# Kernel tuning notes

Hardware: AMD Instinct MI355X
Metric: run time of the kernel (lower is better)

## Reference

```python
import jax, jax.numpy as jnp
import numpy as np

B, S, D, P = 8, 2048, 512, 64  # batch, seq, num_embed_hidden, num_attention_project


def setup_inputs() -> dict:
    key = jax.random.key(0)
    ks = jax.random.split(key, 9)
    sd = 1.0 / np.sqrt(D)
    sp = 1.0 / np.sqrt(P)
    return {
        "query": jax.random.normal(ks[0], (B, S, D), dtype=jnp.float32),
        "attention_mask": jnp.ones((B, S), dtype=jnp.float32),
        "Wq": jax.random.uniform(ks[1], (D, P), jnp.float32, -sd, sd),
        "bq": jax.random.uniform(ks[2], (P,), jnp.float32, -sd, sd),
        "Wk": jax.random.uniform(ks[3], (D, P), jnp.float32, -sd, sd),
        "bk": jax.random.uniform(ks[4], (P,), jnp.float32, -sd, sd),
        "Wv": jax.random.uniform(ks[5], (D, P), jnp.float32, -sd, sd),
        "bv": jax.random.uniform(ks[6], (P,), jnp.float32, -sd, sd),
        "Wo": jax.random.uniform(ks[7], (P, D), jnp.float32, -sp, sp),
        "bo": jax.random.uniform(ks[8], (D,), jnp.float32, -sp, sp),
    }


def reference(query, attention_mask, Wq, bq, Wk, bk, Wv, bv, Wo, bo):
    q = jnp.einsum("bsd,dp->bsp", query, Wq) + bq  # [B,S,P]
    k = jnp.einsum("bsd,dp->bsp", query, Wk) + bk
    v = jnp.einsum("bsd,dp->bsp", query, Wv) + bv
    scores = jnp.einsum("bsp,btp->bst", q, k) / jnp.sqrt(jnp.float32(P))  # [B,S,S]
    # Faithful to original: mask broadcast over last axis via unsqueeze(-1) -> masks rows
    scores = scores + (1.0 - attention_mask[:, :, None]) * -10000.0
    weights = jax.nn.softmax(scores, axis=-1)
    weighted = jnp.einsum("bst,btp->bsp", weights, v)
    return jnp.einsum("bsp,pd->bsd", weighted, Wo) + bo
```

## Files before the change

### kernel.cpp

```cpp
#include <hip/hip_runtime.h>
#include <hip/hip_bf16.h>
#include <math.h>

constexpr int B = 8;
constexpr int S = 2048;
constexpr int D = 512;
constexpr int P = 64;
constexpr float SCALE = 0.125f;

typedef short bf16x8 __attribute__((ext_vector_type(8)));
typedef float f32x4 __attribute__((ext_vector_type(4)));
typedef unsigned int u32;

__device__ __forceinline__ unsigned short f2bf(float x) {
  __hip_bfloat16 h = __float2bfloat16(x);
  return __builtin_bit_cast(unsigned short, h);
}
__device__ __forceinline__ float bf2f(unsigned short u) {
  unsigned int v = (unsigned int)u << 16;
  return __builtin_bit_cast(float, v);
}

__device__ __forceinline__ void ld_g2lds16(const unsigned short* g,
                                           unsigned short* l) {
  __builtin_amdgcn_global_load_lds(
      (const __attribute__((address_space(1))) u32*)g,
      (__attribute__((address_space(3))) u32*)l, 16, 0, 0);
}

__global__ __launch_bounds__(256) void prep_w(
    const float* __restrict__ Wq, const float* __restrict__ Wk,
    const float* __restrict__ Wv, const float* __restrict__ Wo,
    unsigned short* __restrict__ WcatT, unsigned short* __restrict__ WoT) {
  const int i = blockIdx.x * 256 + threadIdx.x;
  if (i < 192 * 512) {
    const int n = i >> 9, k = i & 511;
    const float* W = (n < 64) ? Wq : (n < 128) ? Wk : Wv;
    WcatT[i] = f2bf(W[k * 64 + (n & 63)]);
  }
  if (i < 512 * 64) {
    WoT[i] = f2bf(Wo[(i & 63) * 512 + (i >> 6)]);
  }
}

__global__ __launch_bounds__(256) void qkv_mfma(
    const float* __restrict__ query, const unsigned short* __restrict__ WcatT,
    const float* __restrict__ bq, const float* __restrict__ bk,
    const float* __restrict__ bv, unsigned short* __restrict__ q_bf,
    unsigned short* __restrict__ k_bf, unsigned short* __restrict__ vT_bf) {
  __shared__ __align__(16) unsigned short Aq[64 * 512];
  __shared__ __align__(16) unsigned short Bb[192 * 64];

  const int tid = threadIdx.x;
  const int w = tid >> 6;
  const int l = tid & 63;
  const int l15 = l & 15;
  const int l4 = l >> 4;
  const int s0 = blockIdx.x * 64;

  const float* qsrc = query + (size_t)s0 * D;
  for (int step = 0; step < 16; ++step) {
    const int row = step * 4 + w;
    const float* pf = qsrc + row * D + l * 8;
    const float4 x = *(const float4*)pf;
    const float4 y = *(const float4*)(pf + 4);
    bf16x8 u;
    u[0] = (short)f2bf(x.x); u[1] = (short)f2bf(x.y);
    u[2] = (short)f2bf(x.z); u[3] = (short)f2bf(x.w);
    u[4] = (short)f2bf(y.x); u[5] = (short)f2bf(y.y);
    u[6] = (short)f2bf(y.z); u[7] = (short)f2bf(y.w);
    *(bf16x8*)&Aq[row * 512 + ((l ^ (row & 7)) << 3)] = u;
  }

  f32x4 acc[4][3];
#pragma unroll
  for (int st = 0; st < 4; ++st)
#pragma unroll
    for (int nt = 0; nt < 3; ++nt) acc[st][nt] = (f32x4){0.f, 0.f, 0.f, 0.f};

  const int wn = w * 48;

  for (int kc = 0; kc < 8; ++kc) {
#pragma unroll
    for (int c = 0; c < 6; ++c) {
      const int n = c * 32 + w * 8 + (l >> 3);
      const unsigned short* gp =
          WcatT + (size_t)n * 512 + kc * 64 + (((l & 7) ^ (l >> 3)) << 3);
      ld_g2lds16(gp, &Bb[(c * 256 + w * 64) * 8]);
    }
    __syncthreads();

#pragma unroll
    for (int kk = 0; kk < 2; ++kk) {
      bf16x8 af[4], bfr[3];
#pragma unroll
      for (int st = 0; st < 4; ++st) {
        const int row = st * 16 + l15;
        const int slot = (kc * 8 + kk * 4 + l4) ^ (row & 7);
        af[st] = *(const bf16x8*)&Aq[row * 512 + (slot << 3)];
      }
#pragma unroll
      for (int nt = 0; nt < 3; ++nt) {
        const int n = wn + nt * 16 + l15;
        const int slot = (kk * 4 + l4) ^ (n & 7);
        bfr[nt] = *(const bf16x8*)&Bb[n * 64 + (slot << 3)];
      }
#pragma unroll
      for (int st = 0; st < 4; ++st)
#pragma unroll
        for (int nt = 0; nt < 3; ++nt)
          acc[st][nt] = __builtin_amdgcn_mfma_f32_16x16x32_bf16(
              af[st], bfr[nt], acc[st][nt], 0, 0, 0);
    }
    __syncthreads();
  }

  const int batch = s0 >> 11;
  const int sloc = s0 & 2047;
#pragma unroll
  for (int st = 0; st < 4; ++st) {
#pragma unroll
    for (int nt = 0; nt < 3; ++nt) {
      const int col = wn + nt * 16 + l15;
      const int mat = col >> 6;
      const int p = col & 63;
      const float bb = ((mat == 0) ? bq : (mat == 1) ? bk : bv)[p];
#pragma unroll
      for (int r = 0; r < 4; ++r) {
        const int row = st * 16 + l4 * 4 + r;
        const float vl = acc[st][nt][r] + bb;
        if (mat == 0)
          q_bf[(size_t)(s0 + row) * P + p] = f2bf(vl * SCALE);
        else if (mat == 1)
          k_bf[(size_t)(s0 + row) * P + p] = f2bf(vl);
        else
          vT_bf[((size_t)batch * P + p) * S + sloc + row] = f2bf(vl);
      }
    }
  }
}

__global__ __launch_bounds__(256) void attn(
    const unsigned short* __restrict__ q_bf,
    const unsigned short* __restrict__ k_bf,
    const unsigned short* __restrict__ vT_bf,
    unsigned short* __restrict__ wout) {
  __shared__ __align__(16) unsigned short e_lds[4][2][16 * 32];
  __shared__ __align__(16) float wacc_lds[4][32 * 64];
  __shared__ float l_lds[4][32];

  const int tid = threadIdx.x;
  const int w = tid >> 6;
  const int lane = tid & 63;
  const int l15 = lane & 15;
  const int l4 = lane >> 4;

  const int blk = blockIdx.x;
  const int b = blk & 7;
  const int qt = blk >> 3;
  const int s0 = qt * 32;

  const unsigned short* qb = q_bf + ((size_t)b * S + s0) * P;
  const unsigned short* kb = k_bf + (size_t)b * S * P;
  const unsigned short* vtb = vT_bf + (size_t)b * P * S;

  bf16x8 aq[2][2];
#pragma unroll
  for (int st = 0; st < 2; ++st)
#pragma unroll
    for (int h = 0; h < 2; ++h)
      aq[st][h] =
          *(const bf16x8*)(qb + (size_t)(st * 16 + l15) * P + h * 32 + l4 * 8);

  f32x4 acc[2][4];
#pragma unroll
  for (int st = 0; st < 2; ++st)
#pragma unroll
    for (int pc = 0; pc < 4; ++pc) acc[st][pc] = (f32x4){0.f, 0.f, 0.f, 0.f};
  float lpart[2][4] = {{0.f, 0.f, 0.f, 0.f}, {0.f, 0.f, 0.f, 0.f}};

  for (int win = 0; win < 16; ++win) {
    const int t0 = w * 512 + win * 32;

    bf16x8 bk[2][2];
#pragma unroll
    for (int tile = 0; tile < 2; ++tile)
#pragma unroll
      for (int h = 0; h < 2; ++h)
        bk[tile][h] = *(const bf16x8*)(kb +
                                       (size_t)(t0 + tile * 16 + l15) * P +
                                       h * 32 + l4 * 8);

#pragma unroll
    for (int st = 0; st < 2; ++st) {
#pragma unroll
      for (int tile = 0; tile < 2; ++tile) {
        f32x4 c = (f32x4){0.f, 0.f, 0.f, 0.f};
        c = __builtin_amdgcn_mfma_f32_16x16x32_bf16(aq[st][0], bk[tile][0], c,
                                                    0, 0, 0);
        c = __builtin_amdgcn_mfma_f32_16x16x32_bf16(aq[st][1], bk[tile][1], c,
                                                    0, 0, 0);
#pragma unroll
        for (int r = 0; r < 4; ++r) {
          const unsigned short eu = f2bf(__expf(c[r]));
          lpart[st][r] += bf2f(eu);
          e_lds[w][st][(l4 * 4 + r) * 32 + tile * 16 + l15] = eu;
        }
      }
    }

#pragma unroll
    for (int st = 0; st < 2; ++st) {
      const bf16x8 ae = *(const bf16x8*)&e_lds[w][st][l15 * 32 + l4 * 8];
#pragma unroll
      for (int pc = 0; pc < 4; ++pc) {
        const bf16x8 bv = *(const bf16x8*)(vtb +
                                           (size_t)(pc * 16 + l15) * S + t0 +
                                           l4 * 8);
        acc[st][pc] =
            __builtin_amdgcn_mfma_f32_16x16x32_bf16(ae, bv, acc[st][pc], 0, 0,
                                                    0);
      }
    }
  }

#pragma unroll
  for (int st = 0; st < 2; ++st) {
#pragma unroll
    for (int r = 0; r < 4; ++r) {
      float v = lpart[st][r];
      v += __shfl_xor(v, 1, 64);
      v += __shfl_xor(v, 2, 64);
      v += __shfl_xor(v, 4, 64);
      v += __shfl_xor(v, 8, 64);
      if (l15 == 0) l_lds[w][st * 16 + l4 * 4 + r] = v;
    }
  }

#pragma unroll
  for (int st = 0; st < 2; ++st)
#pragma unroll
    for (int pc = 0; pc < 4; ++pc)
#pragma unroll
      for (int r = 0; r < 4; ++r)
        wacc_lds[w][(st * 16 + l4 * 4 + r) * 64 + pc * 16 + l15] =
            acc[st][pc][r];
  __syncthreads();

  for (int i = tid; i < 32 * 64; i += 256) {
    const int row = i >> 6;
    const int p = i & 63;
    float s = 0.f, ls = 0.f;
#pragma unroll
    for (int ww = 0; ww < 4; ++ww) {
      s += wacc_lds[ww][row * 64 + p];
      ls += l_lds[ww][row];
    }
    wout[((size_t)b * S + s0 + row) * P + p] = f2bf(s / ls);
  }
}

__global__ __launch_bounds__(256) void out_mfma(
    const unsigned short* __restrict__ wtd,
    const unsigned short* __restrict__ WoT,
    const float* __restrict__ bo, float* __restrict__ out) {
  __shared__ __align__(16) unsigned short Aw[64 * 64];
  __shared__ __align__(16) unsigned short Bo[128 * 64];

  const int tid = threadIdx.x;
  const int w = tid >> 6;
  const int l = tid & 63;
  const int l15 = l & 15;
  const int l4 = l >> 4;
  const int s0 = (blockIdx.x >> 2) * 64;
  const int nb = (blockIdx.x & 3) * 128;

#pragma unroll
  for (int c = 0; c < 2; ++c) {
    const int row = c * 32 + w * 8 + (l >> 3);
    const unsigned short* gp =
        wtd + (size_t)(s0 + row) * 64 + (((l & 7) ^ (l >> 3)) << 3);
    ld_g2lds16(gp, &Aw[(c * 256 + w * 64) * 8]);
  }
#pragma unroll
  for (int c = 0; c < 4; ++c) {
    const int n = c * 32 + w * 8 + (l >> 3);
    const unsigned short* gp =
        WoT + (size_t)(nb + n) * 64 + (((l & 7) ^ (l >> 3)) << 3);
    ld_g2lds16(gp, &Bo[(c * 256 + w * 64) * 8]);
  }
  __syncthreads();

  f32x4 acc[4][2];
#pragma unroll
  for (int st = 0; st < 4; ++st)
#pragma unroll
    for (int nt = 0; nt < 2; ++nt) acc[st][nt] = (f32x4){0.f, 0.f, 0.f, 0.f};

#pragma unroll
  for (int kk = 0; kk < 2; ++kk) {
    bf16x8 af[4], bfr[2];
#pragma unroll
    for (int st = 0; st < 4; ++st) {
      const int row = st * 16 + l15;
      const int slot = (kk * 4 + l4) ^ (row & 7);
      af[st] = *(const bf16x8*)&Aw[row * 64 + (slot << 3)];
    }
#pragma unroll
    for (int nt = 0; nt < 2; ++nt) {
      const int n = w * 32 + nt * 16 + l15;
      const int slot = (kk * 4 + l4) ^ (n & 7);
      bfr[nt] = *(const bf16x8*)&Bo[n * 64 + (slot << 3)];
    }
#pragma unroll
    for (int st = 0; st < 4; ++st)
#pragma unroll
      for (int nt = 0; nt < 2; ++nt)
        acc[st][nt] = __builtin_amdgcn_mfma_f32_16x16x32_bf16(
            af[st], bfr[nt], acc[st][nt], 0, 0, 0);
  }

#pragma unroll
  for (int st = 0; st < 4; ++st) {
#pragma unroll
    for (int nt = 0; nt < 2; ++nt) {
      const int col = nb + w * 32 + nt * 16 + l15;
      const float bb = bo[col];
#pragma unroll
      for (int r = 0; r < 4; ++r) {
        const int row = st * 16 + l4 * 4 + r;
        out[(size_t)(s0 + row) * D + col] = acc[st][nt][r] + bb;
      }
    }
  }
}

extern "C" void kernel_launch(void* const* d_in, const int* in_sizes, int n_in,
                              void* d_out, int out_size, void* d_ws,
                              size_t ws_size, hipStream_t stream) {
  const float* query = (const float*)d_in[0];
  const float* Wq = (const float*)d_in[2];
  const float* bq = (const float*)d_in[3];
  const float* Wk = (const float*)d_in[4];
  const float* bk = (const float*)d_in[5];
  const float* Wv = (const float*)d_in[6];
  const float* bv = (const float*)d_in[7];
  const float* Wo = (const float*)d_in[8];
  const float* bo = (const float*)d_in[9];
  float* out = (float*)d_out;

  const size_t n_rows = (size_t)B * S;
  const size_t proj = n_rows * P;
  unsigned short* qbf = (unsigned short*)d_ws;
  unsigned short* kbf = qbf + proj;
  unsigned short* vtbf = kbf + proj;
  unsigned short* wtd = vtbf + proj;
  unsigned short* WcatT = wtd + proj;
  unsigned short* WoT = WcatT + 192 * 512;

  prep_w<<<384, 256, 0, stream>>>(Wq, Wk, Wv, Wo, WcatT, WoT);
  qkv_mfma<<<256, 256, 0, stream>>>(query, WcatT, bq, bk, bv, qbf, kbf, vtbf);
  attn<<<512, 256, 0, stream>>>(qbf, kbf, vtbf, wtd);
  out_mfma<<<1024, 256, 0, stream>>>(wtd, WoT, bo, out);
}
```

Measured before the change: 151.2 us.

## Fuse output projection into attention and retile QKV projection kernel

Merges the output-projection GEMM into the attention kernel, so the normalized weighted values are written to LDS as bf16 and multiplied by WoT in the same block. This drops the intermediate global buffer and one launch. The attention kernel now handles 16 query rows per block (1024 blocks), swizzles the exp tile in LDS and prefetches the next K window into registers. The QKV kernel uses 32-row tiles with 512 blocks and reads weights straight from global memory instead of staging them through LDS. Each attention block now rereads all of WoT, and removing the weight staging adds uncached global traffic.

```diff
diff --git a/kernel.cpp b/kernel.cpp
--- a/kernel.cpp
+++ b/kernel.cpp
@@ -19,13 +19,6 @@
 __device__ __forceinline__ float bf2f(unsigned short u) {
   unsigned int v = (unsigned int)u << 16;
   return __builtin_bit_cast(float, v);
-}
-
-__device__ __forceinline__ void ld_g2lds16(const unsigned short* g,
-                                           unsigned short* l) {
-  __builtin_amdgcn_global_load_lds(
-      (const __attribute__((address_space(1))) u32*)g,
-      (__attribute__((address_space(3))) u32*)l, 16, 0, 0);
 }
 
 __global__ __launch_bounds__(256) void prep_w(
@@ -43,23 +36,22 @@
   }
 }
 
-__global__ __launch_bounds__(256) void qkv_mfma(
+__global__ __launch_bounds__(256, 2) void qkv_mfma(
     const float* __restrict__ query, const unsigned short* __restrict__ WcatT,
     const float* __restrict__ bq, const float* __restrict__ bk,
     const float* __restrict__ bv, unsigned short* __restrict__ q_bf,
     unsigned short* __restrict__ k_bf, unsigned short* __restrict__ vT_bf) {
-  __shared__ __align__(16) unsigned short Aq[64 * 512];
-  __shared__ __align__(16) unsigned short Bb[192 * 64];
+  __shared__ __align__(16) unsigned short Aq[32 * 512];
 
   const int tid = threadIdx.x;
   const int w = tid >> 6;
   const int l = tid & 63;
   const int l15 = l & 15;
   const int l4 = l >> 4;
-  const int s0 = blockIdx.x * 64;
+  const int s0 = blockIdx.x * 32;
 
   const float* qsrc = query + (size_t)s0 * D;
-  for (int step = 0; step < 16; ++step) {
+  for (int step = 0; step < 8; ++step) {
     const int row = step * 4 + w;
     const float* pf = qsrc + row * D + l * 8;
     const float4 x = *(const float4*)pf;
@@ -71,54 +63,47 @@
     u[6] = (short)f2bf(y.z); u[7] = (short)f2bf(y.w);
     *(bf16x8*)&Aq[row * 512 + ((l ^ (row & 7)) << 3)] = u;
   }
-
-  f32x4 acc[4][3];
-#pragma unroll
-  for (int st = 0; st < 4; ++st)
+  __syncthreads();
+
+  f32x4 acc[2][3];
+#pragma unroll
+  for (int st = 0; st < 2; ++st)
 #pragma unroll
     for (int nt = 0; nt < 3; ++nt) acc[st][nt] = (f32x4){0.f, 0.f, 0.f, 0.f};
 
   const int wn = w * 48;
 
+#pragma unroll
   for (int kc = 0; kc < 8; ++kc) {
 #pragma unroll
-    for (int c = 0; c < 6; ++c) {
-      const int n = c * 32 + w * 8 + (l >> 3);
-      const unsigned short* gp =
-          WcatT + (size_t)n * 512 + kc * 64 + (((l & 7) ^ (l >> 3)) << 3);
-      ld_g2lds16(gp, &Bb[(c * 256 + w * 64) * 8]);
-    }
-    __syncthreads();
-
-#pragma unroll
     for (int kk = 0; kk < 2; ++kk) {
-      bf16x8 af[4], bfr[3];
-#pragma unroll
-      for (int st = 0; st < 4; ++st) {
+      bf16x8 bfr[3];
+#pragma unroll
+      for (int nt = 0; nt < 3; ++nt) {
+        const int n = wn + nt * 16 + l15;
+        bfr[nt] = *(const bf16x8*)(WcatT + (size_t)n * 512 + kc * 64 +
+                                   kk * 32 + l4 * 8);
+      }
+      bf16x8 af[2];
+#pragma unroll
+      for (int st = 0; st < 2; ++st) {
         const int row = st * 16 + l15;
         const int slot = (kc * 8 + kk * 4 + l4) ^ (row & 7);
         af[st] = *(const bf16x8*)&Aq[row * 512 + (slot << 3)];
       }
 #pragma unroll
-      for (int nt = 0; nt < 3; ++nt) {
-        const int n = wn + nt * 16 + l15;
-        const int slot = (kk * 4 + l4) ^ (n & 7);
-        bfr[nt] = *(const bf16x8*)&Bb[n * 64 + (slot << 3)];
-      }
-#pragma unroll
-      for (int st = 0; st < 4; ++st)
+      for (int st = 0; st < 2; ++st)
 #pragma unroll
         for (int nt = 0; nt < 3; ++nt)
           acc[st][nt] = __builtin_amdgcn_mfma_f32_16x16x32_bf16(
               af[st], bfr[nt], acc[st][nt], 0, 0, 0);
     }
-    __syncthreads();
   }
 
   const int batch = s0 >> 11;
   const int sloc = s0 & 2047;
 #pragma unroll
-  for (int st = 0; st < 4; ++st) {
+  for (int st = 0; st < 2; ++st) {
 #pragma unroll
     for (int nt = 0; nt < 3; ++nt) {
       const int col = wn + nt * 16 + l15;
@@ -140,14 +125,16 @@
   }
 }
 
-__global__ __launch_bounds__(256) void attn(
+__global__ __launch_bounds__(256, 4) void attn_fused(
     const unsigned short* __restrict__ q_bf,
     const unsigned short* __restrict__ k_bf,
     const unsigned short* __restrict__ vT_bf,
-    unsigned short* __restrict__ wout) {
-  __shared__ __align__(16) unsigned short e_lds[4][2][16 * 32];
-  __shared__ __align__(16) float wacc_lds[4][32 * 64];
-  __shared__ float l_lds[4][32];
+    const unsigned short* __restrict__ WoT, const float* __restrict__ bo,
+    float* __restrict__ out) {
+  __shared__ __align__(16) unsigned short e_lds[4][16 * 32];
+  __shared__ __align__(16) float wacc[4][16 * 64];
+  __shared__ float l_lds[4][16];
+  __shared__ __align__(16) unsigned short wnorm[16 * 72];
 
   const int tid = threadIdx.x;
   const int w = tid >> 6;
@@ -157,181 +144,132 @@
 
   const int blk = blockIdx.x;
   const int b = blk & 7;
-  const int qt = blk >> 3;
-  const int s0 = qt * 32;
-
-  const unsigned short* qb = q_bf + ((size_t)b * S + s0) * P;
+  const int s0q = (blk >> 3) * 16;
+
+  const unsigned short* qb = q_bf + ((size_t)b * S + s0q) * P;
   const unsigned short* kb = k_bf + (size_t)b * S * P;
   const unsigned short* vtb = vT_bf + (size_t)b * P * S;
 
-  bf16x8 aq[2][2];
-#pragma unroll
-  for (int st = 0; st < 2; ++st)
+  bf16x8 aq[2];
+#pragma unroll
+  for (int h = 0; h < 2; ++h)
+    aq[h] = *(const bf16x8*)(qb + (size_t)l15 * P + h * 32 + l4 * 8);
+
+  f32x4 acc[4];
+#pragma unroll
+  for (int pc = 0; pc < 4; ++pc) acc[pc] = (f32x4){0.f, 0.f, 0.f, 0.f};
+  float lpart[4] = {0.f, 0.f, 0.f, 0.f};
+
+  const int t0w = w * 512;
+
+  bf16x8 bk_c[2][2];
+#pragma unroll
+  for (int tile = 0; tile < 2; ++tile)
 #pragma unroll
     for (int h = 0; h < 2; ++h)
-      aq[st][h] =
-          *(const bf16x8*)(qb + (size_t)(st * 16 + l15) * P + h * 32 + l4 * 8);
-
-  f32x4 acc[2][4];
-#pragma unroll
-  for (int st = 0; st < 2; ++st)
-#pragma unroll
-    for (int pc = 0; pc < 4; ++pc) acc[st][pc] = (f32x4){0.f, 0.f, 0.f, 0.f};
-  float lpart[2][4] = {{0.f, 0.f, 0.f, 0.f}, {0.f, 0.f, 0.f, 0.f}};
+      bk_c[tile][h] = *(const bf16x8*)(kb + (size_t)(t0w + tile * 16 + l15) * P +
+                                       h * 32 + l4 * 8);
 
   for (int win = 0; win < 16; ++win) {
-    const int t0 = w * 512 + win * 32;
-
-    bf16x8 bk[2][2];
+    const int t0 = t0w + win * 32;
+    const int t0n = t0w + ((win + 1) & 15) * 32;
+
+    bf16x8 bv_c[4];
+#pragma unroll
+    for (int pc = 0; pc < 4; ++pc)
+      bv_c[pc] = *(const bf16x8*)(vtb + (size_t)(pc * 16 + l15) * S + t0 +
+                                  l4 * 8);
+    bf16x8 bk_n[2][2];
 #pragma unroll
     for (int tile = 0; tile < 2; ++tile)
 #pragma unroll
       for (int h = 0; h < 2; ++h)
-        bk[tile][h] = *(const bf16x8*)(kb +
-                                       (size_t)(t0 + tile * 16 + l15) * P +
-                                       h * 32 + l4 * 8);
-
-#pragma unroll
-    for (int st = 0; st < 2; ++st) {
-#pragma unroll
-      for (int tile = 0; tile < 2; ++tile) {
-        f32x4 c = (f32x4){0.f, 0.f, 0.f, 0.f};
-        c = __builtin_amdgcn_mfma_f32_16x16x32_bf16(aq[st][0], bk[tile][0], c,
-                                                    0, 0, 0);
-        c = __builtin_amdgcn_mfma_f32_16x16x32_bf16(aq[st][1], bk[tile][1], c,
-                                                    0, 0, 0);
-#pragma unroll
-        for (int r = 0; r < 4; ++r) {
-          const unsigned short eu = f2bf(__expf(c[r]));
-          lpart[st][r] += bf2f(eu);
-          e_lds[w][st][(l4 * 4 + r) * 32 + tile * 16 + l15] = eu;
-        }
+        bk_n[tile][h] = *(const bf16x8*)(kb +
+                                         (size_t)(t0n + tile * 16 + l15) * P +
+                                         h * 32 + l4 * 8);
+
+#pragma unroll
+    for (int tile = 0; tile < 2; ++tile) {
+      f32x4 c = (f32x4){0.f, 0.f, 0.f, 0.f};
+      c = __builtin_amdgcn_mfma_f32_16x16x32_bf16(aq[0], bk_c[tile][0], c, 0,
+                                                  0, 0);
+      c = __builtin_amdgcn_mfma_f32_16x16x32_bf16(aq[1], bk_c[tile][1], c, 0,
+                                                  0, 0);
+      const int ch = tile * 2 + (l15 >> 3);
+#pragma unroll
+      for (int r = 0; r < 4; ++r) {
+        const int rr = l4 * 4 + r;
+        const unsigned short eu = f2bf(__expf(c[r]));
+        lpart[r] += bf2f(eu);
+        e_lds[w][rr * 32 + ((ch ^ (rr & 3)) << 3) + (l15 & 7)] = eu;
       }
     }
 
-#pragma unroll
-    for (int st = 0; st < 2; ++st) {
-      const bf16x8 ae = *(const bf16x8*)&e_lds[w][st][l15 * 32 + l4 * 8];
-#pragma unroll
-      for (int pc = 0; pc < 4; ++pc) {
-        const bf16x8 bv = *(const bf16x8*)(vtb +
-                                           (size_t)(pc * 16 + l15) * S + t0 +
-                                           l4 * 8);
-        acc[st][pc] =
-            __builtin_amdgcn_mfma_f32_16x16x32_bf16(ae, bv, acc[st][pc], 0, 0,
-                                                    0);
-      }
-    }
-  }
-
-#pragma unroll
-  for (int st = 0; st < 2; ++st) {
-#pragma unroll
-    for (int r = 0; r < 4; ++r) {
-      float v = lpart[st][r];
-      v += __shfl_xor(v, 1, 64);
-      v += __shfl_xor(v, 2, 64);
-      v += __shfl_xor(v, 4, 64);
-      v += __shfl_xor(v, 8, 64);
-      if (l15 == 0) l_lds[w][st * 16 + l4 * 4 + r] = v;
-    }
-  }
-
-#pragma unroll
-  for (int st = 0; st < 2; ++st)
+    const bf16x8 ae =
+        *(const bf16x8*)&e_lds[w][l15 * 32 + ((l4 ^ (l15 & 3)) << 3)];
 #pragma unroll
     for (int pc = 0; pc < 4; ++pc)
-#pragma unroll
-      for (int r = 0; r < 4; ++r)
-        wacc_lds[w][(st * 16 + l4 * 4 + r) * 64 + pc * 16 + l15] =
-            acc[st][pc][r];
+      acc[pc] = __builtin_amdgcn_mfma_f32_16x16x32_bf16(ae, bv_c[pc], acc[pc],
+                                                        0, 0, 0);
+
+#pragma unroll
+    for (int tile = 0; tile < 2; ++tile)
+#pragma unroll
+      for (int h = 0; h < 2; ++h) bk_c[tile][h] = bk_n[tile][h];
+  }
+
+#pragma unroll
+  for (int r = 0; r < 4; ++r) {
+    float v = lpart[r];
+    v += __shfl_xor(v, 1, 64);
+    v += __shfl_xor(v, 2, 64);
+    v += __shfl_xor(v, 4, 64);
+    v += __shfl_xor(v, 8, 64);
+    if (l15 == 0) l_lds[w][l4 * 4 + r] = v;
+  }
+
+#pragma unroll
+  for (int pc = 0; pc < 4; ++pc)
+#pragma unroll
+    for (int r = 0; r < 4; ++r)
+      wacc[w][(l4 * 4 + r) * 64 + pc * 16 + l15] = acc[pc][r];
   __syncthreads();
 
-  for (int i = tid; i < 32 * 64; i += 256) {
-    const int row = i >> 6;
-    const int p = i & 63;
-    float s = 0.f, ls = 0.f;
+  {
+    const int row = tid >> 4;
+    const int p0 = (tid & 15) * 4;
+    float4 s = {0.f, 0.f, 0.f, 0.f};
+    float ls = 0.f;
 #pragma unroll
     for (int ww = 0; ww < 4; ++ww) {
-      s += wacc_lds[ww][row * 64 + p];
+      const float4 t = *(const float4*)&wacc[ww][row * 64 + p0];
+      s.x += t.x; s.y += t.y; s.z += t.z; s.w += t.w;
       ls += l_lds[ww][row];
     }
-    wout[((size_t)b * S + s0 + row) * P + p] = f2bf(s / ls);
-  }
-}
-
-__global__ __launch_bounds__(256) void out_mfma(
-    const unsigned short* __restrict__ wtd,
-    const unsigned short* __restrict__ WoT,
-    const float* __restrict__ bo, float* __restrict__ out) {
-  __shared__ __align__(16) unsigned short Aw[64 * 64];
-  __shared__ __align__(16) unsigned short Bo[128 * 64];
-
-  const int tid = threadIdx.x;
-  const int w = tid >> 6;
-  const int l = tid & 63;
-  const int l15 = l & 15;
-  const int l4 = l >> 4;
-  const int s0 = (blockIdx.x >> 2) * 64;
-  const int nb = (blockIdx.x & 3) * 128;
-
-#pragma unroll
-  for (int c = 0; c < 2; ++c) {
-    const int row = c * 32 + w * 8 + (l >> 3);
-    const unsigned short* gp =
-        wtd + (size_t)(s0 + row) * 64 + (((l & 7) ^ (l >> 3)) << 3);
-    ld_g2lds16(gp, &Aw[(c * 256 + w * 64) * 8]);
-  }
-#pragma unroll
-  for (int c = 0; c < 4; ++c) {
-    const int n = c * 32 + w * 8 + (l >> 3);
-    const unsigned short* gp =
-        WoT + (size_t)(nb + n) * 64 + (((l & 7) ^ (l >> 3)) << 3);
-    ld_g2lds16(gp, &Bo[(c * 256 + w * 64) * 8]);
+    const float rcp = 1.f / ls;
+    const u32 u01 = (u32)f2bf(s.x * rcp) | ((u32)f2bf(s.y * rcp) << 16);
+    const u32 u23 = (u32)f2bf(s.z * rcp) | ((u32)f2bf(s.w * rcp) << 16);
+    u32* dst = (u32*)&wnorm[row * 72 + p0];
+    dst[0] = u01;
+    dst[1] = u23;
   }
   __syncthreads();
 
-  f32x4 acc[4][2];
-#pragma unroll
-  for (int st = 0; st < 4; ++st)
-#pragma unroll
-    for (int nt = 0; nt < 2; ++nt) acc[st][nt] = (f32x4){0.f, 0.f, 0.f, 0.f};
-
-#pragma unroll
-  for (int kk = 0; kk < 2; ++kk) {
-    bf16x8 af[4], bfr[2];
-#pragma unroll
-    for (int st = 0; st < 4; ++st) {
-      const int row = st * 16 + l15;
-      const int slot = (kk * 4 + l4) ^ (row & 7);
-      af[st] = *(const bf16x8*)&Aw[row * 64 + (slot << 3)];
-    }
-#pragma unroll
-    for (int nt = 0; nt < 2; ++nt) {
-      const int n = w * 32 + nt * 16 + l15;
-      const int slot = (kk * 4 + l4) ^ (n & 7);
-      bfr[nt] = *(const bf16x8*)&Bo[n * 64 + (slot << 3)];
-    }
-#pragma unroll
-    for (int st = 0; st < 4; ++st)
-#pragma unroll
-      for (int nt = 0; nt < 2; ++nt)
-        acc[st][nt] = __builtin_amdgcn_mfma_f32_16x16x32_bf16(
-            af[st], bfr[nt], acc[st][nt], 0, 0, 0);
-  }
-
-#pragma unroll
-  for (int st = 0; st < 4; ++st) {
-#pragma unroll
-    for (int nt = 0; nt < 2; ++nt) {
-      const int col = nb + w * 32 + nt * 16 + l15;
-      const float bb = bo[col];
-#pragma unroll
-      for (int r = 0; r < 4; ++r) {
-        const int row = st * 16 + l4 * 4 + r;
-        out[(size_t)(s0 + row) * D + col] = acc[st][nt][r] + bb;
-      }
-    }
+  const bf16x8 a0 = *(const bf16x8*)&wnorm[l15 * 72 + l4 * 8];
+  const bf16x8 a1 = *(const bf16x8*)&wnorm[l15 * 72 + 32 + l4 * 8];
+  const size_t orow0 = (size_t)b * S + s0q;
+#pragma unroll
+  for (int nt = 0; nt < 8; ++nt) {
+    const int col = w * 128 + nt * 16 + l15;
+    const bf16x8 b0 = *(const bf16x8*)(WoT + (size_t)col * 64 + l4 * 8);
+    const bf16x8 b1 = *(const bf16x8*)(WoT + (size_t)col * 64 + 32 + l4 * 8);
+    f32x4 c = (f32x4){0.f, 0.f, 0.f, 0.f};
+    c = __builtin_amdgcn_mfma_f32_16x16x32_bf16(a0, b0, c, 0, 0, 0);
+    c = __builtin_amdgcn_mfma_f32_16x16x32_bf16(a1, b1, c, 0, 0, 0);
+    const float bb = bo[col];
+#pragma unroll
+    for (int r = 0; r < 4; ++r)
+      out[(orow0 + l4 * 4 + r) * D + col] = c[r] + bb;
   }
 }
 
@@ -354,12 +292,10 @@
   unsigned short* qbf = (unsigned short*)d_ws;
   unsigned short* kbf = qbf + proj;
   unsigned short* vtbf = kbf + proj;
-  unsigned short* wtd = vtbf + proj;
-  unsigned short* WcatT = wtd + proj;
+  unsigned short* WcatT = vtbf + proj;
   unsigned short* WoT = WcatT + 192 * 512;
 
   prep_w<<<384, 256, 0, stream>>>(Wq, Wk, Wv, Wo, WcatT, WoT);
-  qkv_mfma<<<256, 256, 0, stream>>>(query, WcatT, bq, bk, bv, qbf, kbf, vtbf);
-  attn<<<512, 256, 0, stream>>>(qbf, kbf, vtbf, wtd);
-  out_mfma<<<1024, 256, 0, stream>>>(wtd, WoT, bo, out);
-}
+  qkv_mfma<<<512, 256, 0, stream>>>(query, WcatT, bq, bk, bv, qbf, kbf, vtbf);
+  attn_fused<<<1024, 256, 0, stream>>>(qbf, kbf, vtbf, WoT, bo, out);
+}
```

New measurement: 193.3 us. 1.28x slower.
